# Performance work log

Measured on AMD Instinct MI355X. Metric: run time of the kernel, lower is better.

## Reference

```python
import jax, jax.numpy as jnp
import numpy as np

ALPHA = 0.05          # embed strength (frames in [0,1])
COEF_R, COEF_C = 4, 3 # mid-frequency DCT coefficient that carries the bit


def _dct_mat():
    # 8x8 orthonormal DCT-II matrix
    n = jnp.arange(8, dtype=jnp.float32)
    D = jnp.cos(jnp.pi * (2.0 * n[None, :] + 1.0) * n[:, None] / 16.0) * jnp.sqrt(2.0 / 8.0)
    return D.at[0].multiply(1.0 / jnp.sqrt(2.0))


def rgb_to_yuv(rgb):
    r, g, b = rgb[:, 0:1], rgb[:, 1:2], rgb[:, 2:3]
    y = 0.299 * r + 0.587 * g + 0.114 * b
    u = -0.147 * r - 0.289 * g + 0.436 * b
    v = 0.615 * r - 0.515 * g - 0.1 * b
    return jnp.concatenate([y, u, v], axis=1)


def yuv_to_rgb(yuv):
    y, u, v = yuv[:, 0:1], yuv[:, 1:2], yuv[:, 2:3]
    r = y + 1.14 * v
    g = y - 0.395 * u - 0.581 * v
    b = y + 2.032 * u
    return jnp.concatenate([r, g, b], axis=1)


def lbp_uniform(gray):
    # uniform LBP, P=8, R=1 (integer 8-neighborhood), per-image max-normalized
    B, H, W = gray.shape
    p = jnp.pad(gray, ((0, 0), (1, 1), (1, 1)), mode='edge')
    offs = [(-1, 0), (-1, 1), (0, 1), (1, 1), (1, 0), (1, -1), (0, -1), (-1, -1)]
    neigh = jnp.stack([p[:, 1 + dy:1 + dy + H, 1 + dx:1 + dx + W] for dy, dx in offs], axis=0)
    bits = (neigh >= gray[None]).astype(jnp.float32)          # [8,B,H,W]
    trans = jnp.sum(jnp.abs(bits - jnp.roll(bits, 1, axis=0)), axis=0)
    s = jnp.sum(bits, axis=0)
    code = jnp.where(trans <= 2.0, s, 9.0)
    mx = jnp.max(code, axis=(1, 2), keepdims=True)
    return code / mx                                           # [B,H,W]


def dct_embed(y, watermark, mask):
    # y: [B,H,W] luma; watermark: [L] int bits; mask: [B,H,W] texture strength
    B, H, W = y.shape
    nh, nw = H // 8, W // 8
    D = _dct_mat()
    yb = y.reshape(B, nh, 8, nw, 8).transpose(0, 1, 3, 2, 4)   # [B,nh,nw,8,8]
    coef = jnp.einsum('ij,bhwjk,lk->bhwil', D, yb, D)          # D @ block @ D^T
    strength = mask.reshape(B, nh, 8, nw, 8).mean(axis=(2, 4)) # [B,nh,nw]
    L = watermark.shape[0]
    idx = (jnp.arange(nh * nw) % L).reshape(nh, nw)
    bits = watermark[idx].astype(jnp.float32)                  # [nh,nw]
    delta = ALPHA * strength * (2.0 * bits - 1.0)[None]        # [B,nh,nw]
    coef = coef.at[..., COEF_R, COEF_C].add(delta)
    inv = jnp.einsum('ji,bhwjk,kl->bhwil', D, coef, D)         # D^T @ coef @ D
    return inv.transpose(0, 1, 3, 2, 4).reshape(B, H, W)


def _forward(frame, watermark, sa_w, sa_b, ca_w1, ca_w2):
    # LBP texture features from grayscale
    gray = 0.299 * frame[:, 0] + 0.587 * frame[:, 1] + 0.114 * frame[:, 2]
    lbp = lbp_uniform(gray)[:, None]                           # [B,1,H,W]
    # spatial attention: 7x7 conv over [frame, lbp] -> sigmoid mask
    sa_in = jnp.concatenate([frame, lbp], axis=1)
    mask = jax.nn.sigmoid(
        jax.lax.conv_general_dilated(sa_in, sa_w, (1, 1), 'SAME',
                                     dimension_numbers=('NCHW', 'OIHW', 'NCHW'))
        + sa_b[None, :, None, None])                           # [B,1,H,W]
    # channel attention on YUV
    yuv = rgb_to_yuv(frame)
    pooled = yuv.mean(axis=(2, 3))                             # [B,3]
    scale = jax.nn.sigmoid(jax.nn.relu(pooled @ ca_w1.T) @ ca_w2.T)
    weighted = yuv * scale[:, :, None, None]
    # blockwise DCT watermark embed on Y channel
    y_marked = dct_embed(weighted[:, 0], watermark, mask[:, 0])
    wm_yuv = jnp.concatenate([y_marked[:, None], weighted[:, 1:2], weighted[:, 2:3]], axis=1)
    return yuv_to_rgb(wm_yuv), mask


def setup_inputs() -> dict:
    key = jax.random.key(0)
    k1, k2, k3, k4, k5 = jax.random.split(key, 5)
    B, H, W, L = 16, 512, 512, 64
    frame = jax.random.uniform(k1, (B, 3, H, W), dtype=jnp.float32)
    watermark = jax.random.randint(k2, (L,), 0, 2, dtype=jnp.int32)
    sa_w = jax.random.normal(k3, (1, 4, 7, 7), dtype=jnp.float32) * 0.1
    sa_b = jnp.zeros((1,), dtype=jnp.float32)
    ca_w1 = jax.random.normal(k4, (3, 3), dtype=jnp.float32) * 0.5
    ca_w2 = jax.random.normal(k5, (3, 3), dtype=jnp.float32) * 0.5
    return {"frame": frame, "watermark": watermark, "sa_w": sa_w, "sa_b": sa_b,
            "ca_w1": ca_w1, "ca_w2": ca_w2}


def reference(frame, watermark, sa_w, sa_b, ca_w1, ca_w2):
    return _forward(frame, watermark, sa_w, sa_b, ca_w1, ca_w2)
```

## Files before the change

### kernel.cpp

```cpp
#include <hip/hip_runtime.h>
#include <stdint.h>

#define BB 16
#define HH 512
#define WW 512
#define HWsz (HH*WW)

__device__ __forceinline__ float grayf(float r,float g,float b){
  return __fadd_rn(__fadd_rn(__fmul_rn(0.299f,r),__fmul_rn(0.587f,g)),__fmul_rn(0.114f,b));
}
__device__ __forceinline__ float sigmoidf_(float x){ return 1.0f/(1.0f+expf(-x)); }

__device__ __forceinline__ int lbp_code(float tl,float tc,float tr,
                                        float ml,float c ,float mr,
                                        float bl,float bc,float br){
  int b0 = tc>=c, b1 = tr>=c, b2 = mr>=c, b3 = br>=c;
  int b4 = bc>=c, b5 = bl>=c, b6 = ml>=c, b7 = tl>=c;
  int s = (b0+b1)+(b2+b3)+(b4+b5)+(b6+b7);
  int tr_ = (b0!=b7)+(b1!=b0)+(b2!=b1)+(b3!=b2)+(b4!=b3)+(b5!=b4)+(b6!=b5)+(b7!=b6);
  return (tr_<=2)? s : 9;
}

#define RSTRIDE 520
__global__ __launch_bounds__(256,4) void k_reduce(const float* __restrict__ frame,
     float4* __restrict__ part){
  const int blk = blockIdx.x;
  const int b = blk >> 6;
  const int s = blk & 63;
  const int r0 = s*8;
  const float4* F = (const float4*)(frame + (size_t)b*3*HWsz);
  __shared__ float sg[10*RSTRIDE];
  const int tid = threadIdx.x;
  float sy=0.f, su=0.f, sv=0.f;
  #pragma unroll
  for(int k=0;k<5;k++){
    int j = tid + 256*k;
    int row = j >> 7;
    int c4  = j & 127;
    int gy  = min(max(r0-1+row,0),HH-1);
    int fi  = gy*128 + c4;
    float4 r4 = F[fi];
    float4 g4 = F[65536  + fi];
    float4 b4 = F[131072 + fi];
    float4 gr;
    gr.x = grayf(r4.x,g4.x,b4.x);
    gr.y = grayf(r4.y,g4.y,b4.y);
    gr.z = grayf(r4.z,g4.z,b4.z);
    gr.w = grayf(r4.w,g4.w,b4.w);
    *(float4*)&sg[row*RSTRIDE + 4 + 4*c4] = gr;
    if(c4==0)   sg[row*RSTRIDE + 3]   = gr.x;
    if(c4==127) sg[row*RSTRIDE + 516] = gr.w;
    if(row>=1 && row<=8){
      sy += (gr.x+gr.y)+(gr.z+gr.w);
      float rs_=(r4.x+r4.y)+(r4.z+r4.w), gs_=(g4.x+g4.y)+(g4.z+g4.w), bs_=(b4.x+b4.y)+(b4.z+b4.w);
      su += -0.147f*rs_ - 0.289f*gs_ + 0.436f*bs_;
      sv +=  0.615f*rs_ - 0.515f*gs_ - 0.1f*bs_;
    }
  }
  __syncthreads();
  int cm = 0;
  {
    const float* base = sg + (2*tid + 3);
    float t0=base[0], t1=base[1], t2=base[2], t3=base[3];
    float m0=base[RSTRIDE], m1=base[RSTRIDE+1], m2=base[RSTRIDE+2], m3=base[RSTRIDE+3];
    #pragma unroll
    for(int R=1;R<=8;R++){
      const float* brow = base + (R+1)*RSTRIDE;
      float b0=brow[0], b1=brow[1], b2=brow[2], b3=brow[3];
      cm = max(cm, lbp_code(t0,t1,t2, m0,m1,m2, b0,b1,b2));
      cm = max(cm, lbp_code(t1,t2,t3, m1,m2,m3, b1,b2,b3));
      t0=m0;t1=m1;t2=m2;t3=m3; m0=b0;m1=b1;m2=b2;m3=b3;
    }
  }
  #pragma unroll
  for(int off=32;off>=1;off>>=1){
    sy += __shfl_down(sy,off,64);
    su += __shfl_down(su,off,64);
    sv += __shfl_down(sv,off,64);
    cm = max(cm,__shfl_down(cm,off,64));
  }
  __shared__ float rs[3][4]; __shared__ int rm[4];
  int wave=tid>>6, lane=tid&63;
  if(lane==0){ rs[0][wave]=sy; rs[1][wave]=su; rs[2][wave]=sv; rm[wave]=cm; }
  __syncthreads();
  if(tid==0){
    part[blk] = make_float4((rs[0][0]+rs[0][1])+(rs[0][2]+rs[0][3]),
                            (rs[1][0]+rs[1][1])+(rs[1][2]+rs[1][3]),
                            (rs[2][0]+rs[2][1])+(rs[2][2]+rs[2][3]),
                            (float)max(max(rm[0],rm[1]),max(rm[2],rm[3])));
  }
}

#define SAS 41
__global__ __launch_bounds__(256,6) void k_main(const float* __restrict__ frame,
    const int* __restrict__ wm, const float* __restrict__ sa_w, const float* __restrict__ sa_b,
    const float* __restrict__ ca_w1, const float* __restrict__ ca_w2,
    const float4* __restrict__ part, float* __restrict__ out)
{
  const int b = blockIdx.z;
  const int tx0 = blockIdx.x*32, ty0 = blockIdx.y*32;
  const float* fr = frame + (size_t)b*3*HWsz;
  const float4* F4 = (const float4*)fr;

  __shared__ float sA[4][38][SAS];
  __shared__ float sgt[44];
  __shared__ float sgb[44];
  __shared__ float ssc[4];
  __shared__ float scodetab[12];

  const int tid = threadIdx.x;

  if(tid < 64){
    float4 p4 = part[b*64 + tid];
    float sy=p4.x, su=p4.y, sv=p4.z, cmf=p4.w;
    #pragma unroll
    for(int off=1; off<64; off<<=1){
      sy  += __shfl_xor(sy,  off, 64);
      su  += __shfl_xor(su,  off, 64);
      sv  += __shfl_xor(sv,  off, 64);
      cmf  = fmaxf(cmf, __shfl_xor(cmf, off, 64));
    }
    float mx = fmaxf(cmf, 1.0f);
    float p0 = sy * (1.0f/(float)HWsz);
    float p1 = su * (1.0f/(float)HWsz);
    float p2 = sv * (1.0f/(float)HWsz);
    float h0 = fmaxf(p0*ca_w1[0] + p1*ca_w1[1] + p2*ca_w1[2], 0.0f);
    float h1 = fmaxf(p0*ca_w1[3] + p1*ca_w1[4] + p2*ca_w1[5], 0.0f);
    float h2 = fmaxf(p0*ca_w1[6] + p1*ca_w1[7] + p2*ca_w1[8], 0.0f);
    if(tid < 3){
      float a = h0*ca_w2[tid*3+0] + h1*ca_w2[tid*3+1] + h2*ca_w2[tid*3+2];
      ssc[tid] = sigmoidf_(a);
    }
    if(tid == 3) ssc[3] = sa_b[0];
    if(tid < 10) scodetab[tid] = (float)tid / mx;
  }

  for(int s = tid; s < 400; s += 256){
    int ly = s / 10;
    int k  = s - ly*10;
    int gy = ty0 + ly - 4;
    int ry = min(max(gy,0),HH-1);
    int gx0 = tx0 + 4*k - 4;
    bool xin = (gx0 >= 0) && (gx0 <= WW-4);
    float4 r4, g4, b4;
    if(xin){
      int fi = ry*(WW/4) + (gx0>>2);
      r4 = F4[fi]; g4 = F4[65536 + fi]; b4 = F4[131072 + fi];
    } else {
      int cc = (gx0 < 0) ? 0 : (WW-1);
      float r = fr[ry*WW+cc], g = fr[HWsz+ry*WW+cc], bl = fr[2*HWsz+ry*WW+cc];
      r4 = make_float4(r,r,r,r); g4 = make_float4(g,g,g,g); b4 = make_float4(bl,bl,bl,bl);
    }
    float gr0 = grayf(r4.x,g4.x,b4.x), gr1 = grayf(r4.y,g4.y,b4.y),
          gr2 = grayf(r4.z,g4.z,b4.z), gr3 = grayf(r4.w,g4.w,b4.w);
    int cbase = 4*k;
    float* gp = (ly==0) ? &sgt[cbase] : ((ly==39) ? &sgb[cbase] : &sA[3][ly-1][cbase]);
    gp[0]=gr0; gp[1]=gr1; gp[2]=gr2; gp[3]=gr3;
    if(ly >= 1 && ly <= 38){
      float z = ((gy >= 0) && (gy < HH) && xin) ? 1.0f : 0.0f;
      float* rp = &sA[0][ly-1][cbase];
      rp[0]          =r4.x*z; rp[1]          =r4.y*z; rp[2]          =r4.z*z; rp[3]          =r4.w*z;
      rp[38*SAS+0]   =g4.x*z; rp[38*SAS+1]   =g4.y*z; rp[38*SAS+2]   =g4.z*z; rp[38*SAS+3]   =g4.w*z;
      rp[2*38*SAS+0] =b4.x*z; rp[2*38*SAS+1] =b4.y*z; rp[2*38*SAS+2] =b4.z*z; rp[2*38*SAS+3] =b4.w*z;
    }
  }
  __syncthreads();

  float lv[2][4];
  #pragma unroll
  for(int it=0; it<2; ++it){
    int s2 = tid + 256*it;
    if(s2 < 380){
      int lr = s2 / 10;
      int q  = s2 - lr*10;
      int lx0 = 4*q;
      const float* rowM = &sA[3][lr][0];
      const float* rowT = (lr==0)  ? sgt : &sA[3][lr-1][0];
      const float* rowB = (lr==37) ? sgb : &sA[3][lr+1][0];
      float t_[6], m_[6], b_[6];
      #pragma unroll
      for(int j=0;j<6;j++){
        int c = lx0 - 1 + j;
        t_[j]=rowT[c]; m_[j]=rowM[c]; b_[j]=rowB[c];
      }
      int gy = ty0 + lr - 3;
      bool rowin = (gy >= 0) && (gy < HH);
      #pragma unroll
      for(int j=0;j<4;j++){
        int lx = lx0 + j;
        int gx = tx0 + lx - 4;
        float v = 0.0f;
        if(rowin && lx >= 1 && lx <= 38 && gx >= 0 && gx < WW){
          float c = m_[j+1];
          int msk = ((t_[j+1]>=c)?1:0)   | ((t_[j+2]>=c)?2:0)  | ((m_[j+2]>=c)?4:0) |
                    ((b_[j+2]>=c)?8:0)   | ((b_[j+1]>=c)?16:0) | ((b_[j]>=c)?32:0)  |
                    ((m_[j]>=c)?64:0)    | ((t_[j]>=c)?128:0);
          int s8  = __popc(msk);
          int rot = ((msk<<1) | (msk>>7)) & 255;
          int tr_ = __popc(msk ^ rot);
          int code = (tr_ <= 2) ? s8 : 9;
          v = scodetab[code];
        }
        lv[it][j] = v;
      }
    }
  }
  __syncthreads();
  #pragma unroll
  for(int it=0; it<2; ++it){
    int s2 = tid + 256*it;
    if(s2 < 380){
      int lr = s2 / 10;
      int q  = s2 - lr*10;
      float* wp2 = &sA[3][lr][4*q];
      wp2[0]=lv[it][0]; wp2[1]=lv[it][1]; wp2[2]=lv[it][2]; wp2[3]=lv[it][3];
    }
  }
  __syncthreads();

  const int t  = tid & 7;
  const int ty = tid >> 3;
  float a0=ssc[3], a1=ssc[3], a2=ssc[3], a3=ssc[3];
  for(int ci=0;ci<4;ci++){
    #pragma unroll
    for(int ky=0;ky<7;ky++){
      const float* rowp = &sA[ci][ty+ky][4*t];
      float win[10];
      #pragma unroll
      for(int w=0;w<10;w++) win[w]=rowp[1+w];
      const float* wr = &sa_w[ci*49 + ky*7];
      #pragma unroll
      for(int kx=0;kx<7;kx++){
        float wt = wr[kx];
        a0 += win[kx+0]*wt;
        a1 += win[kx+1]*wt;
        a2 += win[kx+2]*wt;
        a3 += win[kx+3]*wt;
      }
    }
  }
  float m0=sigmoidf_(a0), m1=sigmoidf_(a1), m2=sigmoidf_(a2), m3=sigmoidf_(a3);
  {
    size_t midx = (size_t)(3*BB)*HWsz + (size_t)b*HWsz + (size_t)(ty0+ty)*WW + (size_t)(tx0+4*t);
    *reinterpret_cast<float4*>(out + midx) = make_float4(m0,m1,m2,m3);
  }

  float partl = (m0+m1)+(m2+m3);
  partl += __shfl_xor(partl, 1, 64);
  partl += __shfl_xor(partl, 8, 64);
  partl += __shfl_xor(partl, 16, 64);
  partl += __shfl_xor(partl, 32, 64);
  const float strength = partl * (1.0f/64.0f);

  {
    const float sc0=ssc[0], sc1=ssc[1], sc2=ssc[2];
    const int bw = (tx0 + 4*t) >> 3;
    const float sgn = (float)(2*wm[bw]-1);
    const float d4 = (((ty+1)&2) ? -0.35355339059327373f : 0.35355339059327373f);
    const float delta = 0.05f * strength * sgn * d4;
    const float D3tab[8] = { 0.4157348061512726f,-0.0975451610080641f,-0.4903926402016152f,-0.2777851165098011f,
                             0.2777851165098011f, 0.4903926402016152f, 0.0975451610080641f,-0.4157348061512726f };
    float vr[4], vg[4], vb[4];
    #pragma unroll
    for(int j=0;j<4;j++){
      float r  = sA[0][ty+3][4*t+j+4];
      float g  = sA[1][ty+3][4*t+j+4];
      float bl = sA[2][ty+3][4*t+j+4];
      float yv = (0.299f*r + 0.587f*g + 0.114f*bl) * sc0;
      float uv = (-0.147f*r - 0.289f*g + 0.436f*bl) * sc1;
      float vv = ( 0.615f*r - 0.515f*g - 0.1f*bl) * sc2;
      float ym = yv + delta * D3tab[(t&1)*4 + j];
      vr[j] = ym + 1.14f*vv;
      vg[j] = ym - 0.395f*uv - 0.581f*vv;
      vb[j] = ym + 2.032f*uv;
    }
    size_t base = (size_t)(ty0+ty)*WW + (size_t)(tx0+4*t);
    *reinterpret_cast<float4*>(out + (size_t)(b*3+0)*HWsz + base) = make_float4(vr[0],vr[1],vr[2],vr[3]);
    *reinterpret_cast<float4*>(out + (size_t)(b*3+1)*HWsz + base) = make_float4(vg[0],vg[1],vg[2],vg[3]);
    *reinterpret_cast<float4*>(out + (size_t)(b*3+2)*HWsz + base) = make_float4(vb[0],vb[1],vb[2],vb[3]);
  }
}

extern "C" void kernel_launch(void* const* d_in, const int* in_sizes, int n_in,
                              void* d_out, int out_size, void* d_ws, size_t ws_size,
                              hipStream_t stream) {
  const float* frame = (const float*)d_in[0];
  const int*   wmark = (const int*)d_in[1];
  const float* sa_w  = (const float*)d_in[2];
  const float* sa_b  = (const float*)d_in[3];
  const float* ca_w1 = (const float*)d_in[4];
  const float* ca_w2 = (const float*)d_in[5];
  float* out = (float*)d_out;
  float4* part = (float4*)d_ws;

  hipLaunchKernelGGL(k_reduce, dim3(1024),      dim3(256), 0, stream, frame, part);
  hipLaunchKernelGGL(k_main,   dim3(16,16,16),  dim3(256), 0, stream, frame, wmark, sa_w, sa_b, ca_w1, ca_w2, part, out);
}
```

Baseline: 152.3 us.

## Store LBP codes as bytes in reduce pass and reuse them in main kernel

```diff
diff --git a/kernel.cpp b/kernel.cpp
--- a/kernel.cpp
+++ b/kernel.cpp
@@ -23,7 +23,7 @@
 
 #define RSTRIDE 520
 __global__ __launch_bounds__(256,4) void k_reduce(const float* __restrict__ frame,
-     float4* __restrict__ part){
+     float4* __restrict__ part, unsigned short* __restrict__ codes16){
   const int blk = blockIdx.x;
   const int b = blk >> 6;
   const int s = blk & 63;
@@ -67,8 +67,11 @@
     for(int R=1;R<=8;R++){
       const float* brow = base + (R+1)*RSTRIDE;
       float b0=brow[0], b1=brow[1], b2=brow[2], b3=brow[3];
-      cm = max(cm, lbp_code(t0,t1,t2, m0,m1,m2, b0,b1,b2));
-      cm = max(cm, lbp_code(t1,t2,t3, m1,m2,m3, b1,b2,b3));
+      int c1 = lbp_code(t0,t1,t2, m0,m1,m2, b0,b1,b2);
+      int c2 = lbp_code(t1,t2,t3, m1,m2,m3, b1,b2,b3);
+      cm = max(cm, max(c1,c2));
+      codes16[(size_t)b*(HWsz/2) + (size_t)(r0+R-1)*(WW/2) + tid] =
+          (unsigned short)(c1 | (c2<<8));
       t0=m0;t1=m1;t2=m2;t3=m3; m0=b0;m1=b1;m2=b2;m3=b3;
     }
   }
@@ -95,7 +98,8 @@
 __global__ __launch_bounds__(256,6) void k_main(const float* __restrict__ frame,
     const int* __restrict__ wm, const float* __restrict__ sa_w, const float* __restrict__ sa_b,
     const float* __restrict__ ca_w1, const float* __restrict__ ca_w2,
-    const float4* __restrict__ part, float* __restrict__ out)
+    const float4* __restrict__ part, const unsigned char* __restrict__ codes8,
+    float* __restrict__ out)
 {
   const int b = blockIdx.z;
   const int tx0 = blockIdx.x*32, ty0 = blockIdx.y*32;
@@ -103,118 +107,70 @@
   const float4* F4 = (const float4*)fr;
 
   __shared__ float sA[4][38][SAS];
-  __shared__ float sgt[44];
-  __shared__ float sgb[44];
   __shared__ float ssc[4];
-  __shared__ float scodetab[12];
 
   const int tid = threadIdx.x;
 
-  if(tid < 64){
-    float4 p4 = part[b*64 + tid];
-    float sy=p4.x, su=p4.y, sv=p4.z, cmf=p4.w;
-    #pragma unroll
-    for(int off=1; off<64; off<<=1){
-      sy  += __shfl_xor(sy,  off, 64);
-      su  += __shfl_xor(su,  off, 64);
-      sv  += __shfl_xor(sv,  off, 64);
-      cmf  = fmaxf(cmf, __shfl_xor(cmf, off, 64));
-    }
-    float mx = fmaxf(cmf, 1.0f);
-    float p0 = sy * (1.0f/(float)HWsz);
-    float p1 = su * (1.0f/(float)HWsz);
-    float p2 = sv * (1.0f/(float)HWsz);
-    float h0 = fmaxf(p0*ca_w1[0] + p1*ca_w1[1] + p2*ca_w1[2], 0.0f);
-    float h1 = fmaxf(p0*ca_w1[3] + p1*ca_w1[4] + p2*ca_w1[5], 0.0f);
-    float h2 = fmaxf(p0*ca_w1[6] + p1*ca_w1[7] + p2*ca_w1[8], 0.0f);
-    if(tid < 3){
-      float a = h0*ca_w2[tid*3+0] + h1*ca_w2[tid*3+1] + h2*ca_w2[tid*3+2];
-      ssc[tid] = sigmoidf_(a);
-    }
-    if(tid == 3) ssc[3] = sa_b[0];
-    if(tid < 10) scodetab[tid] = (float)tid / mx;
-  }
-
-  for(int s = tid; s < 400; s += 256){
-    int ly = s / 10;
-    int k  = s - ly*10;
-    int gy = ty0 + ly - 4;
-    int ry = min(max(gy,0),HH-1);
+  float inv_mx;
+  {
+    float4 p4 = part[b*64 + (tid & 63)];
+    float cmf = p4.w;
+    #pragma unroll
+    for(int off=1; off<64; off<<=1) cmf = fmaxf(cmf, __shfl_xor(cmf, off, 64));
+    inv_mx = 1.0f / fmaxf(cmf, 1.0f);
+    if(tid < 64){
+      float sy=p4.x, su=p4.y, sv=p4.z;
+      #pragma unroll
+      for(int off=1; off<64; off<<=1){
+        sy += __shfl_xor(sy, off, 64);
+        su += __shfl_xor(su, off, 64);
+        sv += __shfl_xor(sv, off, 64);
+      }
+      float p0 = sy * (1.0f/(float)HWsz);
+      float p1 = su * (1.0f/(float)HWsz);
+      float p2 = sv * (1.0f/(float)HWsz);
+      float h0 = fmaxf(p0*ca_w1[0] + p1*ca_w1[1] + p2*ca_w1[2], 0.0f);
+      float h1 = fmaxf(p0*ca_w1[3] + p1*ca_w1[4] + p2*ca_w1[5], 0.0f);
+      float h2 = fmaxf(p0*ca_w1[6] + p1*ca_w1[7] + p2*ca_w1[8], 0.0f);
+      if(tid < 3){
+        float a = h0*ca_w2[tid*3+0] + h1*ca_w2[tid*3+1] + h2*ca_w2[tid*3+2];
+        ssc[tid] = sigmoidf_(a);
+      }
+      if(tid == 3) ssc[3] = sa_b[0];
+    }
+  }
+
+  for(int s = tid; s < 380; s += 256){
+    int lyA = s / 10;
+    int k   = s - lyA*10;
+    int gy  = ty0 + lyA - 3;
+    int ry  = min(max(gy,0),HH-1);
     int gx0 = tx0 + 4*k - 4;
-    bool xin = (gx0 >= 0) && (gx0 <= WW-4);
-    float4 r4, g4, b4;
+    bool xin   = (gx0 >= 0) && (gx0 <= WW-4);
+    bool rowin = (gy >= 0) && (gy < HH);
+    float4 r4 = make_float4(0.f,0.f,0.f,0.f), g4 = r4, b4 = r4;
+    unsigned int cw = 0u;
     if(xin){
       int fi = ry*(WW/4) + (gx0>>2);
       r4 = F4[fi]; g4 = F4[65536 + fi]; b4 = F4[131072 + fi];
-    } else {
-      int cc = (gx0 < 0) ? 0 : (WW-1);
-      float r = fr[ry*WW+cc], g = fr[HWsz+ry*WW+cc], bl = fr[2*HWsz+ry*WW+cc];
-      r4 = make_float4(r,r,r,r); g4 = make_float4(g,g,g,g); b4 = make_float4(bl,bl,bl,bl);
-    }
-    float gr0 = grayf(r4.x,g4.x,b4.x), gr1 = grayf(r4.y,g4.y,b4.y),
-          gr2 = grayf(r4.z,g4.z,b4.z), gr3 = grayf(r4.w,g4.w,b4.w);
-    int cbase = 4*k;
-    float* gp = (ly==0) ? &sgt[cbase] : ((ly==39) ? &sgb[cbase] : &sA[3][ly-1][cbase]);
-    gp[0]=gr0; gp[1]=gr1; gp[2]=gr2; gp[3]=gr3;
-    if(ly >= 1 && ly <= 38){
-      float z = ((gy >= 0) && (gy < HH) && xin) ? 1.0f : 0.0f;
-      float* rp = &sA[0][ly-1][cbase];
-      rp[0]          =r4.x*z; rp[1]          =r4.y*z; rp[2]          =r4.z*z; rp[3]          =r4.w*z;
-      rp[38*SAS+0]   =g4.x*z; rp[38*SAS+1]   =g4.y*z; rp[38*SAS+2]   =g4.z*z; rp[38*SAS+3]   =g4.w*z;
-      rp[2*38*SAS+0] =b4.x*z; rp[2*38*SAS+1] =b4.y*z; rp[2*38*SAS+2] =b4.z*z; rp[2*38*SAS+3] =b4.w*z;
-    }
-  }
-  __syncthreads();
-
-  float lv[2][4];
-  #pragma unroll
-  for(int it=0; it<2; ++it){
-    int s2 = tid + 256*it;
-    if(s2 < 380){
-      int lr = s2 / 10;
-      int q  = s2 - lr*10;
-      int lx0 = 4*q;
-      const float* rowM = &sA[3][lr][0];
-      const float* rowT = (lr==0)  ? sgt : &sA[3][lr-1][0];
-      const float* rowB = (lr==37) ? sgb : &sA[3][lr+1][0];
-      float t_[6], m_[6], b_[6];
-      #pragma unroll
-      for(int j=0;j<6;j++){
-        int c = lx0 - 1 + j;
-        t_[j]=rowT[c]; m_[j]=rowM[c]; b_[j]=rowB[c];
-      }
-      int gy = ty0 + lr - 3;
-      bool rowin = (gy >= 0) && (gy < HH);
-      #pragma unroll
-      for(int j=0;j<4;j++){
-        int lx = lx0 + j;
-        int gx = tx0 + lx - 4;
-        float v = 0.0f;
-        if(rowin && lx >= 1 && lx <= 38 && gx >= 0 && gx < WW){
-          float c = m_[j+1];
-          int msk = ((t_[j+1]>=c)?1:0)   | ((t_[j+2]>=c)?2:0)  | ((m_[j+2]>=c)?4:0) |
-                    ((b_[j+2]>=c)?8:0)   | ((b_[j+1]>=c)?16:0) | ((b_[j]>=c)?32:0)  |
-                    ((m_[j]>=c)?64:0)    | ((t_[j]>=c)?128:0);
-          int s8  = __popc(msk);
-          int rot = ((msk<<1) | (msk>>7)) & 255;
-          int tr_ = __popc(msk ^ rot);
-          int code = (tr_ <= 2) ? s8 : 9;
-          v = scodetab[code];
-        }
-        lv[it][j] = v;
-      }
-    }
-  }
-  __syncthreads();
-  #pragma unroll
-  for(int it=0; it<2; ++it){
-    int s2 = tid + 256*it;
-    if(s2 < 380){
-      int lr = s2 / 10;
-      int q  = s2 - lr*10;
-      float* wp2 = &sA[3][lr][4*q];
-      wp2[0]=lv[it][0]; wp2[1]=lv[it][1]; wp2[2]=lv[it][2]; wp2[3]=lv[it][3];
-    }
+      if(rowin)
+        cw = *reinterpret_cast<const unsigned int*>(codes8 + (size_t)b*HWsz + (size_t)gy*WW + gx0);
+    }
+    float z = (rowin && xin) ? 1.0f : 0.0f;
+    int cb = 4*k;
+    float* rp = &sA[0][lyA][cb];
+    rp[0]          =r4.x*z; rp[1]          =r4.y*z; rp[2]          =r4.z*z; rp[3]          =r4.w*z;
+    rp[38*SAS+0]   =g4.x*z; rp[38*SAS+1]   =g4.y*z; rp[38*SAS+2]   =g4.z*z; rp[38*SAS+3]   =g4.w*z;
+    rp[2*38*SAS+0] =b4.x*z; rp[2*38*SAS+1] =b4.y*z; rp[2*38*SAS+2] =b4.z*z; rp[2*38*SAS+3] =b4.w*z;
+    float l0 = (float)(cw      & 255u) * inv_mx;
+    float l1 = (float)((cw>>8) & 255u) * inv_mx;
+    float l2 = (float)((cw>>16)& 255u) * inv_mx;
+    float l3 = (float)((cw>>24)& 255u) * inv_mx;
+    float* lp = &sA[3][lyA][cb];
+    lp[0] = (cb   >= 1 ) ? l0 : 0.0f;
+    lp[1] = l1;
+    lp[2] = l2;
+    lp[3] = (cb+3 <= 38) ? l3 : 0.0f;
   }
   __syncthreads();
 
@@ -291,8 +247,11 @@
   const float* ca_w1 = (const float*)d_in[4];
   const float* ca_w2 = (const float*)d_in[5];
   float* out = (float*)d_out;
-  float4* part = (float4*)d_ws;
-
-  hipLaunchKernelGGL(k_reduce, dim3(1024),      dim3(256), 0, stream, frame, part);
-  hipLaunchKernelGGL(k_main,   dim3(16,16,16),  dim3(256), 0, stream, frame, wmark, sa_w, sa_b, ca_w1, ca_w2, part, out);
-}
+  char* ws = (char*)d_ws;
+  float4* part = (float4*)ws;
+  unsigned short* codes16 = (unsigned short*)(ws + 16384);
+  const unsigned char* codes8 = (const unsigned char*)(ws + 16384);
+
+  hipLaunchKernelGGL(k_reduce, dim3(1024),      dim3(256), 0, stream, frame, part, codes16);
+  hipLaunchKernelGGL(k_main,   dim3(16,16,16),  dim3(256), 0, stream, frame, wmark, sa_w, sa_b, ca_w1, ca_w2, part, codes8, out);
+}
```

Result: no change. 151.3 us (-0.7%).
